# Performance work log

Hardware: AMD Instinct MI355X
Metric: run time of the kernel (lower is better)

## Reference

```python
import jax, jax.numpy as jnp
import numpy as np

N, IN_DIM, OUT_DIM = 8192, 256, 64
NEG_BIG = -9e15
LRELU_SLOPE = 0.01  # torch F.leaky_relu default


def setup_inputs() -> dict:
    key = jax.random.key(0)
    k1, k2, k3, k4 = jax.random.split(key, 4)
    inp = jax.random.normal(k1, (N, IN_DIM), dtype=jnp.float32)
    adj = jax.random.randint(k2, (N, N), 0, 2, dtype=jnp.int32)
    # xavier_uniform with gain=1.414
    limW = 1.414 * np.sqrt(6.0 / (IN_DIM + OUT_DIM))
    W = jax.random.uniform(k3, (IN_DIM, OUT_DIM), minval=-limW, maxval=limW, dtype=jnp.float32)
    lima = 1.414 * np.sqrt(6.0 / (2 * OUT_DIM + 1))
    a = jax.random.uniform(k4, (2 * OUT_DIM, 1), minval=-lima, maxval=lima, dtype=jnp.float32)
    return {"input": inp, "adj": adj, "W": W, "a": a}


def reference(input, adj, W, a):
    h = input @ W                      # [N, D]
    a1, a2 = a[:OUT_DIM, 0], a[OUT_DIM:, 0]
    # e[i,j] = leaky_relu(a1.h_i + a2.h_j) == the concat-based score, no NxNx2D tensor
    f1 = h @ a1                        # [N]
    f2 = h @ a2                        # [N]
    e = jax.nn.leaky_relu(f1[:, None] + f2[None, :], negative_slope=LRELU_SLOPE)  # [N, N]
    face_Rhand = e[1, 2]
    face_Lhand = e[1, 3]
    Rhand_Lhand = e[3, 2]
    attention = jnp.where(adj > 0, e, jnp.float32(NEG_BIG))
    alpha = jax.nn.softmax(attention, axis=1)
    h_prime = alpha @ h                # [N, D]
    return (h_prime, face_Rhand, face_Lhand, Rhand_Lhand)
```

## Files before the change

### kernel.cpp

```cpp
#include <hip/hip_runtime.h>
#include <hip/hip_bf16.h>

#define GN 8192
#define KD 256
#define OD 64
#define LOG2E 1.44269504f
#define ASTR 264

typedef __attribute__((ext_vector_type(8))) short bf16x8;
typedef __attribute__((ext_vector_type(4))) float f32x4;

__device__ __forceinline__ float fexp2(float x) {
#if __has_builtin(__builtin_amdgcn_exp2f)
  return __builtin_amdgcn_exp2f(x);
#else
  return exp2f(x);
#endif
}

__global__ __launch_bounds__(256) void gat_k1(
    const float* __restrict__ input, const float* __restrict__ W,
    const float* __restrict__ a, __hip_bfloat16* __restrict__ hT,
    float* __restrict__ f1p, float* __restrict__ f2p, float* __restrict__ out)
{
  __shared__ float Wl[KD * OD];
  __shared__ float inT[KD * 33];
  __shared__ float red1[8][32];
  __shared__ float red2[8][32];
  __shared__ float s1row[32];
  __shared__ float s2row[32];

  const int tid = threadIdx.x;
  const int i0 = blockIdx.x * 32;

  for (int idx = tid; idx < KD * OD / 4; idx += 256)
    ((float4*)Wl)[idx] = ((const float4*)W)[idx];

#pragma unroll
  for (int it = 0; it < 8; ++it) {
    int idx = tid + it * 256;
    int r = idx >> 6, k4 = idx & 63;
    float4 v = *(const float4*)(input + (long)(i0 + r) * KD + k4 * 4);
    inT[(k4 * 4 + 0) * 33 + r] = v.x;
    inT[(k4 * 4 + 1) * 33 + r] = v.y;
    inT[(k4 * 4 + 2) * 33 + r] = v.z;
    inT[(k4 * 4 + 3) * 33 + r] = v.w;
  }
  __syncthreads();

  const int r = tid & 31;
  const int cg = tid >> 5;
  float acc[8];
#pragma unroll
  for (int c = 0; c < 8; ++c) acc[c] = 0.f;

#pragma unroll 4
  for (int k = 0; k < KD; ++k) {
    float inv = inT[k * 33 + r];
    float4 wa = *(const float4*)&Wl[k * 64 + cg * 8];
    float4 wb = *(const float4*)&Wl[k * 64 + cg * 8 + 4];
    acc[0] += inv * wa.x; acc[1] += inv * wa.y;
    acc[2] += inv * wa.z; acc[3] += inv * wa.w;
    acc[4] += inv * wb.x; acc[5] += inv * wb.y;
    acc[6] += inv * wb.z; acc[7] += inv * wb.w;
  }

#pragma unroll
  for (int c = 0; c < 8; ++c)
    hT[(long)(cg * 8 + c) * GN + i0 + r] = __float2bfloat16(acc[c]);

  float s1 = 0.f, s2 = 0.f;
#pragma unroll
  for (int c = 0; c < 8; ++c) {
    s1 += acc[c] * a[cg * 8 + c];
    s2 += acc[c] * a[OD + cg * 8 + c];
  }
  red1[cg][r] = s1; red2[cg][r] = s2;
  __syncthreads();
  if (tid < 32) {
    float f1 = 0.f, f2 = 0.f;
#pragma unroll
    for (int g = 0; g < 8; ++g) { f1 += red1[g][tid]; f2 += red2[g][tid]; }
    s1row[tid] = f1; s2row[tid] = f2;
    f1p[i0 + tid] = f1 * LOG2E;
    f2p[i0 + tid] = f2 * LOG2E;
  }
  __syncthreads();
  if (blockIdx.x == 0 && tid == 0) {
    float e12 = s1row[1] + s2row[2];
    float e13 = s1row[1] + s2row[3];
    float e32 = s1row[3] + s2row[2];
    out[(long)GN * OD + 0] = fmaxf(e12, 0.01f * e12);
    out[(long)GN * OD + 1] = fmaxf(e13, 0.01f * e13);
    out[(long)GN * OD + 2] = fmaxf(e32, 0.01f * e32);
  }
}

__global__ __launch_bounds__(256, 2) void gat_k2(
    const int* __restrict__ adj, const __hip_bfloat16* __restrict__ hT,
    const float* __restrict__ f1p, const float* __restrict__ f2p,
    float* __restrict__ out)
{
  __shared__ int abuf[2][16 * ASTR];
  __shared__ float pb[4][16][68];
  __shared__ float sb[4][16];

  const int tid = threadIdx.x;
  const int lane = tid & 63;
  const int wv = tid >> 6;
  const int tn = lane & 15;
  const int quad = lane >> 4;
  const int i0 = blockIdx.x * 16;

  const int sr = tid >> 4;
  const int sc = (tid & 15) * 4;
  const int* gsrc = adj + (long)(i0 + sr) * GN + sc;

  const float f1r = f1p[i0 + tn];

  const int jo0 = (2 * wv) * 32 + quad * 8;
  const int jo1 = (2 * wv + 1) * 32 + quad * 8;
  const __hip_bfloat16* hbase = hT + (long)tn * GN;

  f32x4 acc[4];
#pragma unroll
  for (int nf = 0; nf < 4; ++nf) acc[nf] = (f32x4){0.f, 0.f, 0.f, 0.f};
  f32x4 accS = (f32x4){0.f, 0.f, 0.f, 0.f};

  bf16x8 ones;
  {
    short ov = (tn == 0) ? (short)0x3F80 : (short)0;
#pragma unroll
    for (int i = 0; i < 8; ++i) ones[i] = ov;
  }

  int4 st[4];
#pragma unroll
  for (int k = 0; k < 4; ++k) st[k] = *(const int4*)(gsrc + 64 * k);
#pragma unroll
  for (int k = 0; k < 4; ++k) *(int4*)&abuf[0][sr * ASTR + sc + 64 * k] = st[k];
  __syncthreads();

  for (int c = 0; c < 32; ++c) {
    const int cur = c & 1, nxt = cur ^ 1;
    if (c < 31) {
#pragma unroll
      for (int k = 0; k < 4; ++k)
        st[k] = *(const int4*)(gsrc + (c + 1) * 256 + 64 * k);
    }

    const int4 a0 = *(const int4*)&abuf[cur][tn * ASTR + jo0];
    const int4 a1 = *(const int4*)&abuf[cur][tn * ASTR + jo0 + 4];
    const int4 a2 = *(const int4*)&abuf[cur][tn * ASTR + jo1];
    const int4 a3 = *(const int4*)&abuf[cur][tn * ASTR + jo1 + 4];
    const float4 f20 = *(const float4*)(f2p + c * 256 + jo0);
    const float4 f21 = *(const float4*)(f2p + c * 256 + jo0 + 4);
    const float4 f22 = *(const float4*)(f2p + c * 256 + jo1);
    const float4 f23 = *(const float4*)(f2p + c * 256 + jo1 + 4);
    bf16x8 B0[4], B1[4];
#pragma unroll
    for (int nf = 0; nf < 4; ++nf) {
      B0[nf] = *(const bf16x8*)(hbase + (long)nf * (16 * GN) + c * 256 + jo0);
      B1[nf] = *(const bf16x8*)(hbase + (long)nf * (16 * GN) + c * 256 + jo1);
    }

    union { bf16x8 v; unsigned u[4]; } w0, w1;
    {
      float e0 = f1r + f20.x, e1 = f1r + f20.y, e2 = f1r + f20.z, e3 = f1r + f20.w;
      float e4 = f1r + f21.x, e5 = f1r + f21.y, e6 = f1r + f21.z, e7 = f1r + f21.w;
      float v0 = fexp2((a0.x > 0) ? fmaxf(e0, 0.01f * e0) : -256.f);
      float v1 = fexp2((a0.y > 0) ? fmaxf(e1, 0.01f * e1) : -256.f);
      float v2 = fexp2((a0.z > 0) ? fmaxf(e2, 0.01f * e2) : -256.f);
      float v3 = fexp2((a0.w > 0) ? fmaxf(e3, 0.01f * e3) : -256.f);
      float v4 = fexp2((a1.x > 0) ? fmaxf(e4, 0.01f * e4) : -256.f);
      float v5 = fexp2((a1.y > 0) ? fmaxf(e5, 0.01f * e5) : -256.f);
      float v6 = fexp2((a1.z > 0) ? fmaxf(e6, 0.01f * e6) : -256.f);
      float v7 = fexp2((a1.w > 0) ? fmaxf(e7, 0.01f * e7) : -256.f);
      w0.u[0] = __builtin_amdgcn_perm(__float_as_uint(v1), __float_as_uint(v0), 0x07060302u);
      w0.u[1] = __builtin_amdgcn_perm(__float_as_uint(v3), __float_as_uint(v2), 0x07060302u);
      w0.u[2] = __builtin_amdgcn_perm(__float_as_uint(v5), __float_as_uint(v4), 0x07060302u);
      w0.u[3] = __builtin_amdgcn_perm(__float_as_uint(v7), __float_as_uint(v6), 0x07060302u);
    }
    {
      float e0 = f1r + f22.x, e1 = f1r + f22.y, e2 = f1r + f22.z, e3 = f1r + f22.w;
      float e4 = f1r + f23.x, e5 = f1r + f23.y, e6 = f1r + f23.z, e7 = f1r + f23.w;
      float v0 = fexp2((a2.x > 0) ? fmaxf(e0, 0.01f * e0) : -256.f);
      float v1 = fexp2((a2.y > 0) ? fmaxf(e1, 0.01f * e1) : -256.f);
      float v2 = fexp2((a2.z > 0) ? fmaxf(e2, 0.01f * e2) : -256.f);
      float v3 = fexp2((a2.w > 0) ? fmaxf(e3, 0.01f * e3) : -256.f);
      float v4 = fexp2((a3.x > 0) ? fmaxf(e4, 0.01f * e4) : -256.f);
      float v5 = fexp2((a3.y > 0) ? fmaxf(e5, 0.01f * e5) : -256.f);
      float v6 = fexp2((a3.z > 0) ? fmaxf(e6, 0.01f * e6) : -256.f);
      float v7 = fexp2((a3.w > 0) ? fmaxf(e7, 0.01f * e7) : -256.f);
      w1.u[0] = __builtin_amdgcn_perm(__float_as_uint(v1), __float_as_uint(v0), 0x07060302u);
      w1.u[1] = __builtin_amdgcn_perm(__float_as_uint(v3), __float_as_uint(v2), 0x07060302u);
      w1.u[2] = __builtin_amdgcn_perm(__float_as_uint(v5), __float_as_uint(v4), 0x07060302u);
      w1.u[3] = __builtin_amdgcn_perm(__float_as_uint(v7), __float_as_uint(v6), 0x07060302u);
    }

#pragma unroll
    for (int nf = 0; nf < 4; ++nf)
      acc[nf] = __builtin_amdgcn_mfma_f32_16x16x32_bf16(w0.v, B0[nf], acc[nf], 0, 0, 0);
    accS = __builtin_amdgcn_mfma_f32_16x16x32_bf16(w0.v, ones, accS, 0, 0, 0);
#pragma unroll
    for (int nf = 0; nf < 4; ++nf)
      acc[nf] = __builtin_amdgcn_mfma_f32_16x16x32_bf16(w1.v, B1[nf], acc[nf], 0, 0, 0);
    accS = __builtin_amdgcn_mfma_f32_16x16x32_bf16(w1.v, ones, accS, 0, 0, 0);

    if (c < 31) {
#pragma unroll
      for (int k = 0; k < 4; ++k)
        *(int4*)&abuf[nxt][sr * ASTR + sc + 64 * k] = st[k];
    }
    __syncthreads();
  }

#pragma unroll
  for (int nf = 0; nf < 4; ++nf)
#pragma unroll
    for (int rg = 0; rg < 4; ++rg)
      pb[wv][quad * 4 + rg][nf * 16 + tn] = acc[nf][rg];
  if (tn == 0) {
#pragma unroll
    for (int rg = 0; rg < 4; ++rg)
      sb[wv][quad * 4 + rg] = accS[rg];
  }
  __syncthreads();
  for (int t = tid; t < 16 * OD; t += 256) {
    int rr = t >> 6, cc = t & 63;
    float num = pb[0][rr][cc] + pb[1][rr][cc] + pb[2][rr][cc] + pb[3][rr][cc];
    float den = sb[0][rr] + sb[1][rr] + sb[2][rr] + sb[3][rr];
    out[(long)(i0 + rr) * OD + cc] = num / den;
  }
}

extern "C" void kernel_launch(void* const* d_in, const int* in_sizes, int n_in,
                              void* d_out, int out_size, void* d_ws, size_t ws_size,
                              hipStream_t stream) {
  const float* input = (const float*)d_in[0];
  const int* adj     = (const int*)d_in[1];
  const float* W     = (const float*)d_in[2];
  const float* a     = (const float*)d_in[3];
  float* out = (float*)d_out;

  __hip_bfloat16* hT = (__hip_bfloat16*)d_ws;
  float* f1p = (float*)((char*)d_ws + (size_t)OD * GN * sizeof(__hip_bfloat16));
  float* f2p = f1p + GN;

  gat_k1<<<256, 256, 0, stream>>>(input, W, a, hT, f1p, f2p, out);
  gat_k2<<<512, 256, 0, stream>>>(adj, hT, f1p, f2p, out);
}
```

Baseline: 392.6 us.

## Split attention columns across two blocks, async adj loads to LDS, prefetch h

Each row group's column range is now split across two blocks, giving 1024 blocks with a higher occupancy hint. Adj tiles are copied straight into LDS with global_load_lds instead of passing through registers, and the next chunk's h fragments are prefetched into registers. Partial numerators and denominators go to workspace and a third kernel combines them and divides. The goal is better latency hiding for the adj memory stream, paid for with an extra launch and extra partial traffic.

```diff
diff --git a/kernel.cpp b/kernel.cpp
--- a/kernel.cpp
+++ b/kernel.cpp
@@ -5,7 +5,8 @@
 #define KD 256
 #define OD 64
 #define LOG2E 1.44269504f
-#define ASTR 264
+#define ASTR 260
+#define NCH 16
 
 typedef __attribute__((ext_vector_type(8))) short bf16x8;
 typedef __attribute__((ext_vector_type(4))) float f32x4;
@@ -16,6 +17,12 @@
 #else
   return exp2f(x);
 #endif
+}
+
+__device__ __forceinline__ void async_cp16(const void* g, void* l) {
+  __builtin_amdgcn_global_load_lds(
+      (const __attribute__((address_space(1))) unsigned int*)g,
+      (__attribute__((address_space(3))) unsigned int*)l, 16, 0, 0);
 }
 
 __global__ __launch_bounds__(256) void gat_k1(
@@ -96,31 +103,36 @@
   }
 }
 
-__global__ __launch_bounds__(256, 2) void gat_k2(
+__global__ __launch_bounds__(256, 4) void gat_k2(
     const int* __restrict__ adj, const __hip_bfloat16* __restrict__ hT,
     const float* __restrict__ f1p, const float* __restrict__ f2p,
-    float* __restrict__ out)
+    float* __restrict__ pn, float* __restrict__ pd)
 {
-  __shared__ int abuf[2][16 * ASTR];
-  __shared__ float pb[4][16][68];
-  __shared__ float sb[4][16];
+  __shared__ int smem[2 * 16 * ASTR];
+  float* pb = (float*)smem;
+  float* sb = pb + 4 * 16 * 68;
 
   const int tid = threadIdx.x;
   const int lane = tid & 63;
   const int wv = tid >> 6;
   const int tn = lane & 15;
   const int quad = lane >> 4;
-  const int i0 = blockIdx.x * 16;
-
-  const int sr = tid >> 4;
-  const int sc = (tid & 15) * 4;
-  const int* gsrc = adj + (long)(i0 + sr) * GN + sc;
+  const int rg = blockIdx.x >> 1;
+  const int js = blockIdx.x & 1;
+  const int i0 = rg * 16;
+  const int jbase = js * 4096;
 
   const float f1r = f1p[i0 + tn];
-
   const int jo0 = (2 * wv) * 32 + quad * 8;
-  const int jo1 = (2 * wv + 1) * 32 + quad * 8;
-  const __hip_bfloat16* hbase = hT + (long)tn * GN;
+  const int jo1 = jo0 + 32;
+  const __hip_bfloat16* hbase = hT + (long)tn * GN + jbase;
+  const float* fpb = f2p + jbase;
+
+  const int srow = wv * 4;
+  const int* g0 = adj + (long)(i0 + srow + 0) * GN + jbase + lane * 4;
+  const int* g1 = adj + (long)(i0 + srow + 1) * GN + jbase + lane * 4;
+  const int* g2 = adj + (long)(i0 + srow + 2) * GN + jbase + lane * 4;
+  const int* g3 = adj + (long)(i0 + srow + 3) * GN + jbase + lane * 4;
 
   f32x4 acc[4];
 #pragma unroll
@@ -134,35 +146,36 @@
     for (int i = 0; i < 8; ++i) ones[i] = ov;
   }
 
-  int4 st[4];
-#pragma unroll
-  for (int k = 0; k < 4; ++k) st[k] = *(const int4*)(gsrc + 64 * k);
-#pragma unroll
-  for (int k = 0; k < 4; ++k) *(int4*)&abuf[0][sr * ASTR + sc + 64 * k] = st[k];
-  __syncthreads();
-
-  for (int c = 0; c < 32; ++c) {
-    const int cur = c & 1, nxt = cur ^ 1;
-    if (c < 31) {
-#pragma unroll
-      for (int k = 0; k < 4; ++k)
-        st[k] = *(const int4*)(gsrc + (c + 1) * 256 + 64 * k);
-    }
-
-    const int4 a0 = *(const int4*)&abuf[cur][tn * ASTR + jo0];
-    const int4 a1 = *(const int4*)&abuf[cur][tn * ASTR + jo0 + 4];
-    const int4 a2 = *(const int4*)&abuf[cur][tn * ASTR + jo1];
-    const int4 a3 = *(const int4*)&abuf[cur][tn * ASTR + jo1 + 4];
-    const float4 f20 = *(const float4*)(f2p + c * 256 + jo0);
-    const float4 f21 = *(const float4*)(f2p + c * 256 + jo0 + 4);
-    const float4 f22 = *(const float4*)(f2p + c * 256 + jo1);
-    const float4 f23 = *(const float4*)(f2p + c * 256 + jo1 + 4);
-    bf16x8 B0[4], B1[4];
-#pragma unroll
-    for (int nf = 0; nf < 4; ++nf) {
-      B0[nf] = *(const bf16x8*)(hbase + (long)nf * (16 * GN) + c * 256 + jo0);
-      B1[nf] = *(const bf16x8*)(hbase + (long)nf * (16 * GN) + c * 256 + jo1);
-    }
+  async_cp16(g0, &smem[(srow + 0) * ASTR]);
+  async_cp16(g1, &smem[(srow + 1) * ASTR]);
+  async_cp16(g2, &smem[(srow + 2) * ASTR]);
+  async_cp16(g3, &smem[(srow + 3) * ASTR]);
+  bf16x8 B0[4], B1[4];
+#pragma unroll
+  for (int nf = 0; nf < 4; ++nf) {
+    B0[nf] = *(const bf16x8*)(hbase + (long)nf * (16 * GN) + jo0);
+    B1[nf] = *(const bf16x8*)(hbase + (long)nf * (16 * GN) + jo1);
+  }
+  __syncthreads();
+
+  for (int c = 0; c < NCH; ++c) {
+    const int cur = (c & 1) * (16 * ASTR);
+    const int nxt = ((c & 1) ^ 1) * (16 * ASTR);
+    if (c + 1 < NCH) {
+      async_cp16(g0 + (c + 1) * 256, &smem[nxt + (srow + 0) * ASTR]);
+      async_cp16(g1 + (c + 1) * 256, &smem[nxt + (srow + 1) * ASTR]);
+      async_cp16(g2 + (c + 1) * 256, &smem[nxt + (srow + 2) * ASTR]);
+      async_cp16(g3 + (c + 1) * 256, &smem[nxt + (srow + 3) * ASTR]);
+    }
+
+    const float4 f20 = *(const float4*)(fpb + c * 256 + jo0);
+    const float4 f21 = *(const float4*)(fpb + c * 256 + jo0 + 4);
+    const float4 f22 = *(const float4*)(fpb + c * 256 + jo1);
+    const float4 f23 = *(const float4*)(fpb + c * 256 + jo1 + 4);
+    const int4 a0 = *(const int4*)&smem[cur + tn * ASTR + jo0];
+    const int4 a1 = *(const int4*)&smem[cur + tn * ASTR + jo0 + 4];
+    const int4 a2 = *(const int4*)&smem[cur + tn * ASTR + jo1];
+    const int4 a3 = *(const int4*)&smem[cur + tn * ASTR + jo1 + 4];
 
     union { bf16x8 v; unsigned u[4]; } w0, w1;
     {
@@ -207,10 +220,12 @@
       acc[nf] = __builtin_amdgcn_mfma_f32_16x16x32_bf16(w1.v, B1[nf], acc[nf], 0, 0, 0);
     accS = __builtin_amdgcn_mfma_f32_16x16x32_bf16(w1.v, ones, accS, 0, 0, 0);
 
-    if (c < 31) {
-#pragma unroll
-      for (int k = 0; k < 4; ++k)
-        *(int4*)&abuf[nxt][sr * ASTR + sc + 64 * k] = st[k];
+    if (c + 1 < NCH) {
+#pragma unroll
+      for (int nf = 0; nf < 4; ++nf) {
+        B0[nf] = *(const bf16x8*)(hbase + (long)nf * (16 * GN) + (c + 1) * 256 + jo0);
+        B1[nf] = *(const bf16x8*)(hbase + (long)nf * (16 * GN) + (c + 1) * 256 + jo1);
+      }
     }
     __syncthreads();
   }
@@ -218,20 +233,35 @@
 #pragma unroll
   for (int nf = 0; nf < 4; ++nf)
 #pragma unroll
-    for (int rg = 0; rg < 4; ++rg)
-      pb[wv][quad * 4 + rg][nf * 16 + tn] = acc[nf][rg];
+    for (int rgi = 0; rgi < 4; ++rgi)
+      pb[(wv * 16 + quad * 4 + rgi) * 68 + nf * 16 + tn] = acc[nf][rgi];
   if (tn == 0) {
 #pragma unroll
-    for (int rg = 0; rg < 4; ++rg)
-      sb[wv][quad * 4 + rg] = accS[rg];
+    for (int rgi = 0; rgi < 4; ++rgi)
+      sb[wv * 16 + quad * 4 + rgi] = accS[rgi];
   }
   __syncthreads();
   for (int t = tid; t < 16 * OD; t += 256) {
     int rr = t >> 6, cc = t & 63;
-    float num = pb[0][rr][cc] + pb[1][rr][cc] + pb[2][rr][cc] + pb[3][rr][cc];
-    float den = sb[0][rr] + sb[1][rr] + sb[2][rr] + sb[3][rr];
-    out[(long)(i0 + rr) * OD + cc] = num / den;
-  }
+    float num = pb[(0 * 16 + rr) * 68 + cc] + pb[(1 * 16 + rr) * 68 + cc] +
+                pb[(2 * 16 + rr) * 68 + cc] + pb[(3 * 16 + rr) * 68 + cc];
+    pn[((long)js * GN + i0 + rr) * OD + cc] = num;
+  }
+  if (tid < 16) {
+    float den = sb[0 * 16 + tid] + sb[1 * 16 + tid] + sb[2 * 16 + tid] + sb[3 * 16 + tid];
+    pd[(long)js * GN + i0 + tid] = den;
+  }
+}
+
+__global__ __launch_bounds__(256) void gat_k3(
+    const float* __restrict__ pn, const float* __restrict__ pd,
+    float* __restrict__ out)
+{
+  long t = (long)blockIdx.x * 256 + threadIdx.x;
+  int i = (int)(t >> 6);
+  float num = pn[t] + pn[(long)GN * OD + t];
+  float den = pd[i] + pd[GN + i];
+  out[t] = num / den;
 }
 
 extern "C" void kernel_launch(void* const* d_in, const int* in_sizes, int n_in,
@@ -243,10 +273,14 @@
   const float* a     = (const float*)d_in[3];
   float* out = (float*)d_out;
 
-  __hip_bfloat16* hT = (__hip_bfloat16*)d_ws;
-  float* f1p = (float*)((char*)d_ws + (size_t)OD * GN * sizeof(__hip_bfloat16));
+  char* ws = (char*)d_ws;
+  __hip_bfloat16* hT = (__hip_bfloat16*)ws;
+  float* f1p = (float*)(ws + (size_t)OD * GN * 2);
   float* f2p = f1p + GN;
+  float* pn  = f2p + GN;
+  float* pd  = pn + (size_t)2 * GN * OD;
 
   gat_k1<<<256, 256, 0, stream>>>(input, W, a, hT, f1p, f2p, out);
-  gat_k2<<<512, 256, 0, stream>>>(adj, hT, f1p, f2p, out);
-}
+  gat_k2<<<1024, 256, 0, stream>>>(adj, hT, f1p, f2p, pn, pd);
+  gat_k3<<<GN * OD / 256, 256, 0, stream>>>(pn, pd, out);
+}
```

Result: slower. 400.8 us (+2.1%).
